# Kernel tuning notes

Measured on AMD Instinct MI355X. Metric: run time of the kernel, lower is better.

## Reference

```python
import jax, jax.numpy as jnp
import numpy as np

N_NODES = 50000
N_EDGES = 800000
IN_DIM = 128
HID = 128
N_GRAPHS = 256


def setup_inputs() -> dict:
    key = jax.random.key(0)
    ks = jax.random.split(key, 12)
    x = jax.random.normal(ks[0], (N_NODES, IN_DIM), dtype=jnp.float32)
    edge_index = jax.random.randint(ks[1], (2, N_EDGES), 0, N_NODES, dtype=jnp.int64)
    batch = jnp.sort(jax.random.randint(ks[2], (N_NODES,), 0, N_GRAPHS, dtype=jnp.int64))
    s = 1.0 / np.sqrt(IN_DIM)
    sh = 1.0 / np.sqrt(HID)
    params = {
        # GraphConv layer 1: out = aggr_add(x_j) @ W_rel + b_rel + x @ W_root
        "w1_rel": jax.random.uniform(ks[3], (IN_DIM, HID), jnp.float32, -s, s),
        "b1_rel": jax.random.uniform(ks[4], (HID,), jnp.float32, -s, s),
        "w1_root": jax.random.uniform(ks[5], (IN_DIM, HID), jnp.float32, -s, s),
        "w2_rel": jax.random.uniform(ks[6], (HID, HID), jnp.float32, -sh, sh),
        "b2_rel": jax.random.uniform(ks[7], (HID,), jnp.float32, -sh, sh),
        "w2_root": jax.random.uniform(ks[8], (HID, HID), jnp.float32, -sh, sh),
        "fc1_w": jax.random.uniform(ks[9], (HID, HID), jnp.float32, -sh, sh),
        "fc1_b": jnp.zeros((HID,), jnp.float32),
        "fc2_w": jax.random.uniform(ks[10], (HID, 1), jnp.float32, -sh, sh),
        "fc2_b": jnp.zeros((1,), jnp.float32),
    }
    return {"x": x, "edge_index": edge_index, "batch": batch, **params}


def _graph_conv(x, src, dst, w_rel, b_rel, w_root):
    # sum-aggregate neighbor features (gather from src, scatter-add to dst)
    agg = jax.ops.segment_sum(x[src], dst, num_segments=N_NODES)
    return agg @ w_rel + b_rel + x @ w_root


def reference(x, edge_index, batch, w1_rel, b1_rel, w1_root,
              w2_rel, b2_rel, w2_root, fc1_w, fc1_b, fc2_w, fc2_b):
    src, dst = edge_index[0], edge_index[1]
    h = jax.nn.relu(_graph_conv(x, src, dst, w1_rel, b1_rel, w1_root))
    h = jax.nn.relu(_graph_conv(h, src, dst, w2_rel, b2_rel, w2_root))
    # global mean pool over graphs in the batch
    sums = jax.ops.segment_sum(h, batch, num_segments=N_GRAPHS)
    counts = jax.ops.segment_sum(jnp.ones((N_NODES,), h.dtype), batch, num_segments=N_GRAPHS)
    pooled = sums / jnp.maximum(counts, 1.0)[:, None]  # [G, HID]
    out = jax.nn.relu(pooled @ fc1_w + fc1_b)
    return out @ fc2_w + fc2_b  # [G, 1]
```

## Files before the change

### kernel.cpp

```cpp
#include <hip/hip_runtime.h>

#define NNODES 50000
#define NEDGES 800000
#define DIM 128
#define NGRAPHS 256
#define NPAD 50176
#define SCAN_BLOCKS 196

typedef _Float16 half4_t __attribute__((ext_vector_type(4)));
typedef _Float16 half8_t __attribute__((ext_vector_type(8)));
typedef float f32x4 __attribute__((ext_vector_type(4)));

__global__ void cast_x_kernel(const float* __restrict__ x, _Float16* __restrict__ xh) {
    int t = blockIdx.x * 256 + threadIdx.x;
    const float4* x4 = reinterpret_cast<const float4*>(x);
    float4 a = x4[t * 2];
    float4 b = x4[t * 2 + 1];
    half8_t h;
    h[0] = (_Float16)a.x; h[1] = (_Float16)a.y; h[2] = (_Float16)a.z; h[3] = (_Float16)a.w;
    h[4] = (_Float16)b.x; h[5] = (_Float16)b.y; h[6] = (_Float16)b.z; h[7] = (_Float16)b.w;
    *reinterpret_cast<half8_t*>(&xh[(size_t)t * 8]) = h;
}

__global__ void cast_w_kernel(const float* __restrict__ w1_rel, const float* __restrict__ w1_root,
                              const float* __restrict__ w2_rel, const float* __restrict__ w2_root,
                              _Float16* __restrict__ WT1, _Float16* __restrict__ WT2) {
    int t = blockIdx.x * 256 + threadIdx.x;
    int layer = t >> 15;
    int r = t & 32767;
    int c = r >> 8;
    int k = r & 255;
    const float* wr = layer ? w2_rel : w1_rel;
    const float* wo = layer ? w2_root : w1_root;
    float v = (k < 128) ? wr[k * DIM + c] : wo[(k - 128) * DIM + c];
    _Float16* dstp = layer ? WT2 : WT1;
    dstp[(size_t)c * 256 + k] = (_Float16)v;
}

__global__ void hist_kernel(const int* __restrict__ dst, int* __restrict__ deg) {
    int e = blockIdx.x * 256 + threadIdx.x;
    if (e < NEDGES) atomicAdd(&deg[dst[e]], 1);
}

__global__ void scan1_kernel(const int* __restrict__ deg, int* __restrict__ bsum) {
    __shared__ int s[256];
    int t = threadIdx.x;
    s[t] = deg[blockIdx.x * 256 + t];
    __syncthreads();
    #pragma unroll
    for (int d = 128; d > 0; d >>= 1) {
        if (t < d) s[t] += s[t + d];
        __syncthreads();
    }
    if (t == 0) bsum[blockIdx.x] = s[0];
}

__global__ void scan2_kernel(int* __restrict__ bsum) {
    __shared__ int s[256];
    int t = threadIdx.x;
    int v = (t < SCAN_BLOCKS) ? bsum[t] : 0;
    s[t] = v;
    __syncthreads();
    #pragma unroll
    for (int d = 1; d < 256; d <<= 1) {
        int u = (t >= d) ? s[t - d] : 0;
        __syncthreads();
        s[t] += u;
        __syncthreads();
    }
    if (t < SCAN_BLOCKS) bsum[t] = (t == 0) ? 0 : s[t - 1];
}

__global__ void scan3_kernel(const int* __restrict__ deg,
                             const int* __restrict__ bsum,
                             int* __restrict__ offs,
                             int* __restrict__ curs) {
    __shared__ int s[256];
    int t = threadIdx.x;
    int idx = blockIdx.x * 256 + t;
    s[t] = deg[idx];
    __syncthreads();
    #pragma unroll
    for (int d = 1; d < 256; d <<= 1) {
        int u = (t >= d) ? s[t - d] : 0;
        __syncthreads();
        s[t] += u;
        __syncthreads();
    }
    int excl = ((t == 0) ? 0 : s[t - 1]) + bsum[blockIdx.x];
    if (idx <= NNODES) {
        offs[idx] = excl;
        curs[idx] = excl;
    }
}

__global__ void bucket_kernel(const int* __restrict__ src,
                              const int* __restrict__ dst,
                              int* __restrict__ curs,
                              int* __restrict__ srcs_sorted) {
    int e = blockIdx.x * 256 + threadIdx.x;
    if (e >= NEDGES) return;
    int pos = atomicAdd(&curs[dst[e]], 1);
    srcs_sorted[pos] = src[e];
}

__global__ void gather_agg_kernel(const _Float16* __restrict__ feat,
                                  const int* __restrict__ offs,
                                  const int* __restrict__ srcs_sorted,
                                  _Float16* __restrict__ agg) {
    int n = blockIdx.x * 8 + (threadIdx.x >> 5);
    int q = threadIdx.x & 31;
    if (n >= NNODES) return;
    int beg = offs[n], end = offs[n + 1];
    float4 a0 = {0.f, 0.f, 0.f, 0.f};
    float4 a1 = {0.f, 0.f, 0.f, 0.f};
    int i = beg;
    for (; i + 2 <= end; i += 2) {
        int s0 = srcs_sorted[i];
        int s1 = srcs_sorted[i + 1];
        half4_t v0 = *reinterpret_cast<const half4_t*>(&feat[(size_t)s0 * DIM + q * 4]);
        half4_t v1 = *reinterpret_cast<const half4_t*>(&feat[(size_t)s1 * DIM + q * 4]);
        a0.x += (float)v0[0]; a0.y += (float)v0[1]; a0.z += (float)v0[2]; a0.w += (float)v0[3];
        a1.x += (float)v1[0]; a1.y += (float)v1[1]; a1.z += (float)v1[2]; a1.w += (float)v1[3];
    }
    if (i < end) {
        half4_t v = *reinterpret_cast<const half4_t*>(&feat[(size_t)srcs_sorted[i] * DIM + q * 4]);
        a0.x += (float)v[0]; a0.y += (float)v[1]; a0.z += (float)v[2]; a0.w += (float)v[3];
    }
    half4_t r;
    r[0] = (_Float16)(a0.x + a1.x);
    r[1] = (_Float16)(a0.y + a1.y);
    r[2] = (_Float16)(a0.z + a1.z);
    r[3] = (_Float16)(a0.w + a1.w);
    *reinterpret_cast<half4_t*>(&agg[(size_t)n * DIM + q * 4]) = r;
}

__global__ __launch_bounds__(256) void conv_mfma_kernel(
        const _Float16* __restrict__ Ah,
        const _Float16* Xh,
        const _Float16* __restrict__ WT,
        const float* __restrict__ bias,
        _Float16* outh) {
    const int wave = threadIdx.x >> 6;
    const int lane = threadIdx.x & 63;
    const int row0 = blockIdx.x * 128 + wave * 32;
    const int rA = lane & 15;
    const int kg = lane >> 4;

    f32x4 acc[2][8];
    #pragma unroll
    for (int m = 0; m < 2; ++m)
        #pragma unroll
        for (int nt = 0; nt < 8; ++nt)
            acc[m][nt] = (f32x4){0.f, 0.f, 0.f, 0.f};

    int ra0 = row0 + rA;        if (ra0 > NNODES - 1) ra0 = NNODES - 1;
    int ra1 = row0 + 16 + rA;   if (ra1 > NNODES - 1) ra1 = NNODES - 1;

    #pragma unroll
    for (int ks = 0; ks < 8; ++ks) {
        const _Float16* srcb = (ks < 4) ? Ah : Xh;
        const int klocal = (ks & 3) * 32 + kg * 8;
        half8_t a0 = *reinterpret_cast<const half8_t*>(&srcb[(size_t)ra0 * DIM + klocal]);
        half8_t a1 = *reinterpret_cast<const half8_t*>(&srcb[(size_t)ra1 * DIM + klocal]);
        const int kglob = ks * 32 + kg * 8;
        #pragma unroll
        for (int nt = 0; nt < 8; ++nt) {
            half8_t b = *reinterpret_cast<const half8_t*>(&WT[(size_t)(nt * 16 + rA) * 256 + kglob]);
            acc[0][nt] = __builtin_amdgcn_mfma_f32_16x16x32_f16(a0, b, acc[0][nt], 0, 0, 0);
            acc[1][nt] = __builtin_amdgcn_mfma_f32_16x16x32_f16(a1, b, acc[1][nt], 0, 0, 0);
        }
    }

    const int ccol = lane & 15;
    const int crow4 = (lane >> 4) * 4;
    #pragma unroll
    for (int m = 0; m < 2; ++m) {
        #pragma unroll
        for (int nt = 0; nt < 8; ++nt) {
            float bb = bias[nt * 16 + ccol];
            #pragma unroll
            for (int r = 0; r < 4; ++r) {
                int row = row0 + m * 16 + crow4 + r;
                if (row < NNODES) {
                    float v = acc[m][nt][r] + bb;
                    outh[(size_t)row * DIM + nt * 16 + ccol] = (_Float16)(v > 0.f ? v : 0.f);
                }
            }
        }
    }
}

__global__ void pool_seg_kernel(const _Float16* __restrict__ h,
                                const int* __restrict__ batch,
                                float* __restrict__ pooled) {
    int g = blockIdx.x;
    int c = threadIdx.x;
    int lo = 0, hi = NNODES;
    while (lo < hi) { int m = (lo + hi) >> 1; if (batch[m] < g) lo = m + 1; else hi = m; }
    int beg = lo;
    hi = NNODES;
    while (lo < hi) { int m = (lo + hi) >> 1; if (batch[m] < g + 1) lo = m + 1; else hi = m; }
    int end = lo;
    float acc0 = 0.f, acc1 = 0.f;
    int n = beg;
    for (; n + 2 <= end; n += 2) {
        acc0 += (float)h[(size_t)n * DIM + c];
        acc1 += (float)h[(size_t)(n + 1) * DIM + c];
    }
    if (n < end) acc0 += (float)h[(size_t)n * DIM + c];
    float cnt = (float)(end - beg);
    pooled[(size_t)g * DIM + c] = (acc0 + acc1) / fmaxf(cnt, 1.f);
}

__global__ void mlp_kernel(const float* __restrict__ pooled,
                           const float* __restrict__ fc1_w,
                           const float* __restrict__ fc1_b,
                           const float* __restrict__ fc2_w,
                           const float* __restrict__ fc2_b,
                           float* __restrict__ out) {
    __shared__ float p[DIM];
    __shared__ float red[DIM];
    int g = blockIdx.x;
    int c = threadIdx.x;
    p[c] = pooled[(size_t)g * DIM + c];
    __syncthreads();
    float acc = fc1_b[c];
    for (int k = 0; k < DIM; ++k) acc = fmaf(p[k], fc1_w[k * DIM + c], acc);
    acc = acc > 0.f ? acc : 0.f;
    red[c] = acc * fc2_w[c];
    __syncthreads();
    #pragma unroll
    for (int s = 64; s > 0; s >>= 1) {
        if (c < s) red[c] += red[c + s];
        __syncthreads();
    }
    if (c == 0) out[g] = red[0] + fc2_b[0];
}

extern "C" void kernel_launch(void* const* d_in, const int* in_sizes, int n_in,
                              void* d_out, int out_size, void* d_ws, size_t ws_size,
                              hipStream_t stream) {
    const float* x       = (const float*)d_in[0];
    const int*   ei      = (const int*)d_in[1];
    const int*   batch   = (const int*)d_in[2];
    const float* w1_rel  = (const float*)d_in[3];
    const float* b1_rel  = (const float*)d_in[4];
    const float* w1_root = (const float*)d_in[5];
    const float* w2_rel  = (const float*)d_in[6];
    const float* b2_rel  = (const float*)d_in[7];
    const float* w2_root = (const float*)d_in[8];
    const float* fc1_w   = (const float*)d_in[9];
    const float* fc1_b   = (const float*)d_in[10];
    const float* fc2_w   = (const float*)d_in[11];
    const float* fc2_b   = (const float*)d_in[12];
    float* out = (float*)d_out;

    char* ws = (char*)d_ws;
    const size_t feath_bytes = (size_t)NNODES * DIM * sizeof(_Float16);
    _Float16* Ah  = (_Float16*)ws;
    _Float16* Hh  = (_Float16*)(ws + feath_bytes);
    _Float16* xh  = (_Float16*)(ws + 2 * feath_bytes);
    _Float16* WT1 = (_Float16*)(ws + 3 * feath_bytes);
    _Float16* WT2 = WT1 + 128 * 256;
    int*   deg    = (int*)(WT2 + 128 * 256);
    int*   offs   = deg + NPAD;
    int*   curs   = offs + NPAD;
    int*   bsum   = curs + NPAD;
    int*   srcs   = bsum + 256;
    float* pooled = (float*)(srcs + NEDGES);

    const int* src = ei;
    const int* dst = ei + NEDGES;

    const int edge_blocks = (NEDGES + 255) / 256;
    const int conv_blocks = (NNODES + 127) / 128;
    const int agg_blocks  = (NNODES + 7) / 8;

    cast_x_kernel<<<(NNODES * DIM / 8) / 256, 256, 0, stream>>>(x, xh);
    cast_w_kernel<<<256, 256, 0, stream>>>(w1_rel, w1_root, w2_rel, w2_root, WT1, WT2);

    hipMemsetAsync(deg, 0, NPAD * sizeof(int), stream);
    hist_kernel<<<edge_blocks, 256, 0, stream>>>(dst, deg);
    scan1_kernel<<<SCAN_BLOCKS, 256, 0, stream>>>(deg, bsum);
    scan2_kernel<<<1, 256, 0, stream>>>(bsum);
    scan3_kernel<<<SCAN_BLOCKS, 256, 0, stream>>>(deg, bsum, offs, curs);
    bucket_kernel<<<edge_blocks, 256, 0, stream>>>(src, dst, curs, srcs);

    gather_agg_kernel<<<agg_blocks, 256, 0, stream>>>(xh, offs, srcs, Ah);
    conv_mfma_kernel<<<conv_blocks, 256, 0, stream>>>(Ah, xh, WT1, b1_rel, Hh);

    gather_agg_kernel<<<agg_blocks, 256, 0, stream>>>(Hh, offs, srcs, Ah);
    conv_mfma_kernel<<<conv_blocks, 256, 0, stream>>>(Ah, Hh, WT2, b2_rel, Hh);

    pool_seg_kernel<<<NGRAPHS, 128, 0, stream>>>(Hh, batch, pooled);
    mlp_kernel<<<NGRAPHS, 128, 0, stream>>>(pooled, fc1_w, fc1_b, fc2_w, fc2_b, out);
}
```

Measured before the change: 353.8 us.

## Widen gather loads to half8 with 4-edge unroll, fuse pool+MLP, nontemporal bucket store

The gather-aggregate kernel now assigns 16 lanes per node, each loading 8 halfs (16-byte vector loads), and unrolls over 4 edges, so more independent gathers are in flight per thread. Pool and MLP kernels are merged into one launch, which drops the pooled intermediate buffer and one kernel launch. The bucket scatter uses a nontemporal store for the sorted source indices. The wider per-thread work raises register use and may reduce occupancy.

```diff
diff --git a/kernel.cpp b/kernel.cpp
--- a/kernel.cpp
+++ b/kernel.cpp
@@ -101,38 +101,44 @@
     int e = blockIdx.x * 256 + threadIdx.x;
     if (e >= NEDGES) return;
     int pos = atomicAdd(&curs[dst[e]], 1);
-    srcs_sorted[pos] = src[e];
+    __builtin_nontemporal_store(src[e], &srcs_sorted[pos]);
 }
 
 __global__ void gather_agg_kernel(const _Float16* __restrict__ feat,
                                   const int* __restrict__ offs,
                                   const int* __restrict__ srcs_sorted,
                                   _Float16* __restrict__ agg) {
-    int n = blockIdx.x * 8 + (threadIdx.x >> 5);
-    int q = threadIdx.x & 31;
+    int n = blockIdx.x * 16 + (threadIdx.x >> 4);
+    int q = threadIdx.x & 15;
     if (n >= NNODES) return;
     int beg = offs[n], end = offs[n + 1];
-    float4 a0 = {0.f, 0.f, 0.f, 0.f};
-    float4 a1 = {0.f, 0.f, 0.f, 0.f};
+    float a0[8] = {0.f, 0.f, 0.f, 0.f, 0.f, 0.f, 0.f, 0.f};
+    float a1[8] = {0.f, 0.f, 0.f, 0.f, 0.f, 0.f, 0.f, 0.f};
     int i = beg;
-    for (; i + 2 <= end; i += 2) {
-        int s0 = srcs_sorted[i];
+    for (; i + 4 <= end; i += 4) {
+        int s0 = srcs_sorted[i + 0];
         int s1 = srcs_sorted[i + 1];
-        half4_t v0 = *reinterpret_cast<const half4_t*>(&feat[(size_t)s0 * DIM + q * 4]);
-        half4_t v1 = *reinterpret_cast<const half4_t*>(&feat[(size_t)s1 * DIM + q * 4]);
-        a0.x += (float)v0[0]; a0.y += (float)v0[1]; a0.z += (float)v0[2]; a0.w += (float)v0[3];
-        a1.x += (float)v1[0]; a1.y += (float)v1[1]; a1.z += (float)v1[2]; a1.w += (float)v1[3];
-    }
-    if (i < end) {
-        half4_t v = *reinterpret_cast<const half4_t*>(&feat[(size_t)srcs_sorted[i] * DIM + q * 4]);
-        a0.x += (float)v[0]; a0.y += (float)v[1]; a0.z += (float)v[2]; a0.w += (float)v[3];
-    }
-    half4_t r;
-    r[0] = (_Float16)(a0.x + a1.x);
-    r[1] = (_Float16)(a0.y + a1.y);
-    r[2] = (_Float16)(a0.z + a1.z);
-    r[3] = (_Float16)(a0.w + a1.w);
-    *reinterpret_cast<half4_t*>(&agg[(size_t)n * DIM + q * 4]) = r;
+        int s2 = srcs_sorted[i + 2];
+        int s3 = srcs_sorted[i + 3];
+        half8_t v0 = *reinterpret_cast<const half8_t*>(&feat[(size_t)s0 * DIM + q * 8]);
+        half8_t v1 = *reinterpret_cast<const half8_t*>(&feat[(size_t)s1 * DIM + q * 8]);
+        half8_t v2 = *reinterpret_cast<const half8_t*>(&feat[(size_t)s2 * DIM + q * 8]);
+        half8_t v3 = *reinterpret_cast<const half8_t*>(&feat[(size_t)s3 * DIM + q * 8]);
+        #pragma unroll
+        for (int j = 0; j < 8; ++j) {
+            a0[j] += (float)v0[j] + (float)v1[j];
+            a1[j] += (float)v2[j] + (float)v3[j];
+        }
+    }
+    for (; i < end; ++i) {
+        half8_t v = *reinterpret_cast<const half8_t*>(&feat[(size_t)srcs_sorted[i] * DIM + q * 8]);
+        #pragma unroll
+        for (int j = 0; j < 8; ++j) a0[j] += (float)v[j];
+    }
+    half8_t r;
+    #pragma unroll
+    for (int j = 0; j < 8; ++j) r[j] = (_Float16)(a0[j] + a1[j]);
+    *reinterpret_cast<half8_t*>(&agg[(size_t)n * DIM + q * 8]) = r;
 }
 
 __global__ __launch_bounds__(256) void conv_mfma_kernel(
@@ -191,9 +197,15 @@
     }
 }
 
-__global__ void pool_seg_kernel(const _Float16* __restrict__ h,
+__global__ void pool_mlp_kernel(const _Float16* __restrict__ h,
                                 const int* __restrict__ batch,
-                                float* __restrict__ pooled) {
+                                const float* __restrict__ fc1_w,
+                                const float* __restrict__ fc1_b,
+                                const float* __restrict__ fc2_w,
+                                const float* __restrict__ fc2_b,
+                                float* __restrict__ out) {
+    __shared__ float p[DIM];
+    __shared__ float red[DIM];
     int g = blockIdx.x;
     int c = threadIdx.x;
     int lo = 0, hi = NNODES;
@@ -210,20 +222,7 @@
     }
     if (n < end) acc0 += (float)h[(size_t)n * DIM + c];
     float cnt = (float)(end - beg);
-    pooled[(size_t)g * DIM + c] = (acc0 + acc1) / fmaxf(cnt, 1.f);
-}
-
-__global__ void mlp_kernel(const float* __restrict__ pooled,
-                           const float* __restrict__ fc1_w,
-                           const float* __restrict__ fc1_b,
-                           const float* __restrict__ fc2_w,
-                           const float* __restrict__ fc2_b,
-                           float* __restrict__ out) {
-    __shared__ float p[DIM];
-    __shared__ float red[DIM];
-    int g = blockIdx.x;
-    int c = threadIdx.x;
-    p[c] = pooled[(size_t)g * DIM + c];
+    p[c] = (acc0 + acc1) / fmaxf(cnt, 1.f);
     __syncthreads();
     float acc = fc1_b[c];
     for (int k = 0; k < DIM; ++k) acc = fmaf(p[k], fc1_w[k * DIM + c], acc);
@@ -268,14 +267,13 @@
     int*   curs   = offs + NPAD;
     int*   bsum   = curs + NPAD;
     int*   srcs   = bsum + 256;
-    float* pooled = (float*)(srcs + NEDGES);
 
     const int* src = ei;
     const int* dst = ei + NEDGES;
 
     const int edge_blocks = (NEDGES + 255) / 256;
     const int conv_blocks = (NNODES + 127) / 128;
-    const int agg_blocks  = (NNODES + 7) / 8;
+    const int agg_blocks  = (NNODES + 15) / 16;
 
     cast_x_kernel<<<(NNODES * DIM / 8) / 256, 256, 0, stream>>>(x, xh);
     cast_w_kernel<<<256, 256, 0, stream>>>(w1_rel, w1_root, w2_rel, w2_root, WT1, WT2);
@@ -293,6 +291,5 @@
     gather_agg_kernel<<<agg_blocks, 256, 0, stream>>>(Hh, offs, srcs, Ah);
     conv_mfma_kernel<<<conv_blocks, 256, 0, stream>>>(Ah, Hh, WT2, b2_rel, Hh);
 
-    pool_seg_kernel<<<NGRAPHS, 128, 0, stream>>>(Hh, batch, pooled);
-    mlp_kernel<<<NGRAPHS, 128, 0, stream>>>(pooled, fc1_w, fc1_b, fc2_w, fc2_b, out);
-}
+    pool_mlp_kernel<<<NGRAPHS, 128, 0, stream>>>(Hh, batch, fc1_w, fc1_b, fc2_w, fc2_b, out);
+}
```

Result: faster. 346.7 us (-2.0%).
